# Performance work log

Measured on AMD Instinct MI355X. Metric: run time of the kernel, lower is better.

The kernel has to match this reference:

```python
import jax, jax.numpy as jnp
import numpy as np

C = 256; HEADS = 16; BS = 8; HS = 3; PS = BS + 2 * HS; G = 32; EPS = 1e-5


def gnorm(x, w, b):
    # GroupNorm(32, C) over any (B, C, *) tensor
    B, Ch = x.shape[0], x.shape[1]
    xs = x.reshape(B, G, -1)
    m = xs.mean(-1, keepdims=True)
    v = xs.var(-1, keepdims=True)
    xs = (xs - m) * jax.lax.rsqrt(v + EPS)
    sh = (1, Ch) + (1,) * (x.ndim - 2)
    return xs.reshape(x.shape) * w.reshape(sh) + b.reshape(sh)


def mha(q, k, v, scale):
    attn = jax.nn.softmax(jnp.einsum('bhid,bhjd->bhij', q, k) * scale, axis=-1)
    return jnp.einsum('bhij,bhjd->bhid', attn, v)


def conv1x1(x, w, b=None):
    y = jnp.einsum('bchw,cd->bdhw', x, w)
    return y if b is None else y + b[None, :, None, None]


def spatial_attn(x, w1, b1, w2, b2, gw, gb):
    wgt = jax.nn.relu(conv1x1(x, w1, b1))
    wgt = jax.nn.sigmoid(conv1x1(wgt, w2, b2))
    return gnorm(x * wgt + x, gw, gb)


def halo_attn(x, qkv_w, proj_w, proj_b):
    B, Ch, H, W = x.shape
    pad_h = (-H) % BS; pad_w = (-W) % BS
    xp = jnp.pad(x, ((0, 0), (0, 0), (HS, pad_h + HS), (HS, pad_w + HS)))
    Hb = (H + pad_h) // BS; Wb = (W + pad_w) // BS
    rows = (np.arange(Hb) * BS)[:, None] + np.arange(PS)  # (Hb, PS)
    cols = (np.arange(Wb) * BS)[:, None] + np.arange(PS)  # (Wb, PS)
    # (B, C, Hb, Wb, PS, PS) halo windows, row-major like F.unfold
    p = xp[:, :, rows[:, None, :, None], cols[None, :, None, :]]
    p = p.transpose(0, 2, 3, 4, 5, 1).reshape(B * Hb * Wb, PS * PS, Ch)
    qkv = p @ qkv_w  # (N, P, 3C)
    d = Ch // HEADS
    qkv = qkv.reshape(-1, PS * PS, 3, HEADS, d).transpose(2, 0, 3, 1, 4)
    q, k, v = qkv[0], qkv[1], qkv[2]  # (N, heads, P, d)
    center = np.array([r * PS + c for r in range(HS, HS + BS) for c in range(HS, HS + BS)])
    q = q[:, :, center, :]  # only center block queries
    o = mha(q, k, v, d ** -0.5)  # (N, heads, BS*BS, d)
    o = o.transpose(0, 2, 1, 3).reshape(-1, BS * BS, Ch) @ proj_w + proj_b
    o = o.reshape(B, Hb, Wb, BS, BS, Ch).transpose(0, 5, 1, 3, 2, 4)
    o = o.reshape(B, Ch, H + pad_h, W + pad_w)
    return o[:, :, :H, :W]


def rot_pass(xn, w):
    B, Ch, H, W = xn.shape
    d = Ch // HEADS
    qkv = conv1x1(xn, w).reshape(B, 3, HEADS, d, H * W)
    q = qkv[:, 0].transpose(0, 1, 3, 2)  # (B, heads, HW, d)
    k = qkv[:, 1].transpose(0, 1, 3, 2)
    v = qkv[:, 2].transpose(0, 1, 3, 2)
    o = mha(q, k, v, d ** -0.5)
    return o.transpose(0, 1, 3, 2).reshape(B, Ch, H, W)


def rotation_attn(x, gw, gb, qkv_w, pw, pb):
    xn = gnorm(x, gw, gb)
    outs = [rot_pass(xn, qkv_w)]
    for k in (1, 2, 3):
        o = rot_pass(jnp.rot90(xn, k, axes=(2, 3)), qkv_w)
        outs.append(jnp.rot90(o, 4 - k, axes=(2, 3)))
    m = jnp.maximum(jnp.maximum(outs[0], outs[1]), jnp.maximum(outs[2], outs[3]))
    return conv1x1(m, pw, pb) + x


def setup_inputs() -> dict:
    key = jax.random.key(0)
    ks = jax.random.split(key, 16)
    B, H, W = 2, 32, 32
    n = lambda k, s: jax.random.normal(k, s, dtype=jnp.float32) * 0.05
    return {
        'x': jax.random.normal(ks[0], (B, C, H, W), dtype=jnp.float32),
        'sa_w1': n(ks[1], (C, C // 8)), 'sa_b1': jnp.zeros((C // 8,), jnp.float32),
        'sa_w2': n(ks[2], (C // 8, C)), 'sa_b2': jnp.zeros((C,), jnp.float32),
        'sa_gn_w': jnp.ones((C,), jnp.float32), 'sa_gn_b': jnp.zeros((C,), jnp.float32),
        'ha_qkv_w': n(ks[3], (C, 3 * C)), 'ha_proj_w': n(ks[4], (C, C)), 'ha_proj_b': jnp.zeros((C,), jnp.float32),
        'ra_gn_w': jnp.ones((C,), jnp.float32), 'ra_gn_b': jnp.zeros((C,), jnp.float32),
        'ra_qkv_w': n(ks[5], (C, 3 * C)), 'ra_proj_w': n(ks[6], (C, C)), 'ra_proj_b': jnp.zeros((C,), jnp.float32),
        'gn_w': jnp.ones((C,), jnp.float32), 'gn_b': jnp.zeros((C,), jnp.float32),
        'toqkv_w': n(ks[7], (C, 3 * C)), 'toqkv_b': jnp.zeros((3 * C,), jnp.float32),
        'attn_weight': jnp.ones((4,), jnp.float32),
        'proj_w': n(ks[8], (C, C)), 'proj_b': jnp.zeros((C,), jnp.float32),
    }


def reference(x, sa_w1, sa_b1, sa_w2, sa_b2, sa_gn_w, sa_gn_b,
              ha_qkv_w, ha_proj_w, ha_proj_b,
              ra_gn_w, ra_gn_b, ra_qkv_w, ra_proj_w, ra_proj_b,
              gn_w, gn_b, toqkv_w, toqkv_b, attn_weight, proj_w, proj_b):
    B, Ch, H, W = x.shape
    d = Ch // HEADS
    sp = spatial_attn(x, sa_w1, sa_b1, sa_w2, sa_b2, sa_gn_w, sa_gn_b)
    ha = halo_attn(x, ha_qkv_w, ha_proj_w, ha_proj_b)
    ro = rotation_attn(x, ra_gn_w, ra_gn_b, ra_qkv_w, ra_proj_w, ra_proj_b)
    # global QKV attention over flattened tokens
    nf = gnorm(x.reshape(B, Ch, H * W), gn_w, gn_b).transpose(0, 2, 1)  # (B, HW, C)
    qkv = nf @ toqkv_w + toqkv_b
    q, k, v = jnp.split(qkv, 3, axis=-1)
    q = q.reshape(B, -1, HEADS, d).transpose(0, 2, 1, 3)
    k = k.reshape(B, -1, HEADS, d).transpose(0, 2, 1, 3)
    v = v.reshape(B, -1, HEADS, d).transpose(0, 2, 1, 3)
    o = mha(q, k, v, d ** -0.5).transpose(0, 2, 1, 3).reshape(B, -1, Ch)
    qo = o.transpose(0, 2, 1).reshape(B, Ch, H, W)
    w4 = jax.nn.softmax(attn_weight)
    comb = sp * w4[0] + ha * w4[1] + qo * w4[2] + ro * w4[3]
    return conv1x1(comb, proj_w, proj_b) + x
```

## Files before the change

### kernel.cpp

```cpp
#include <hip/hip_runtime.h>

#define CC 256
#define HWN 1024
#define EPSV 1e-5f

typedef __attribute__((ext_vector_type(8))) short bf16x8;
typedef __attribute__((ext_vector_type(4))) float f32x4;
typedef __attribute__((ext_vector_type(4))) unsigned short u16x4;

__device__ inline ushort f2bf(float f) {
    union { float f; unsigned u; } v; v.f = f;
    unsigned u = v.u;
    u += 0x7fffu + ((u >> 16) & 1u);
    return (ushort)(u >> 16);
}
__device__ inline void store_out(float* p, float v) { *p = v; }
__device__ inline void store_out(ushort* p, float v) { *p = f2bf(v); }

__global__ __launch_bounds__(256) void k_transpose(const float* __restrict__ in,
                                                   float* __restrict__ out, int R, int Cd) {
    __shared__ float tile[32][33];
    int b = blockIdx.z;
    int r0 = blockIdx.y * 32, c0 = blockIdx.x * 32;
    int tx = threadIdx.x, ty = threadIdx.y;
    const float* inb = in + (size_t)b * R * Cd;
    float* outb = out + (size_t)b * R * Cd;
#pragma unroll
    for (int i = 0; i < 32; i += 8)
        tile[ty + i][tx] = inb[(size_t)(r0 + ty + i) * Cd + c0 + tx];
    __syncthreads();
#pragma unroll
    for (int i = 0; i < 32; i += 8)
        outb[(size_t)(c0 + ty + i) * R + r0 + tx] = tile[tx][ty + i];
}

__global__ __launch_bounds__(256) void k_wtc_all(const float* __restrict__ s0, const float* __restrict__ s1,
                                                 const float* __restrict__ s2, const float* __restrict__ s3,
                                                 const float* __restrict__ s4, const float* __restrict__ s5,
                                                 ushort* __restrict__ d0, ushort* __restrict__ d1,
                                                 ushort* __restrict__ d2, ushort* __restrict__ d3,
                                                 ushort* __restrict__ d4, ushort* __restrict__ d5) {
    __shared__ float tile[32][33];
    int z = blockIdx.z;
    const float* in; ushort* out; int N;
    switch (z) {
        case 0: in = s0; out = d0; N = 768; break;
        case 1: in = s1; out = d1; N = 768; break;
        case 2: in = s2; out = d2; N = 768; break;
        case 3: in = s3; out = d3; N = 256; break;
        case 4: in = s4; out = d4; N = 256; break;
        default: in = s5; out = d5; N = 256; break;
    }
    int n0 = blockIdx.x * 32;
    if (n0 >= N) return;
    int k0 = blockIdx.y * 32;
    int tx = threadIdx.x, ty = threadIdx.y;
#pragma unroll
    for (int i = 0; i < 32; i += 8)
        tile[ty + i][tx] = in[(size_t)(k0 + ty + i) * N + n0 + tx];
    __syncthreads();
#pragma unroll
    for (int i = 0; i < 32; i += 8)
        out[(size_t)(n0 + ty + i) * 256 + k0 + tx] = f2bf(tile[tx][ty + i]);
}

template <typename OT>
__global__ __launch_bounds__(256) void k_mm_bf(const float* __restrict__ A,
                                               const ushort* __restrict__ Wt,
                                               const float* __restrict__ bias,
                                               const float* __restrict__ res,
                                               OT* __restrict__ Cp,
                                               int M, int N, int K) {
    __shared__ __align__(16) ushort As[64][40];
    __shared__ __align__(16) ushort Bs[64][40];
    int tid = threadIdx.x;
    int lane = tid & 63, wid = tid >> 6;
    int wr = (wid >> 1) * 32, wc = (wid & 1) * 32;
    int row0 = blockIdx.y * 64, col0 = blockIdx.x * 64;
    int sr = tid >> 2, skq = (tid & 3) * 8;
    int l16 = lane & 15, kg = (lane >> 4) * 8;
    f32x4 acc[2][2] = {};
    for (int k0 = 0; k0 < K; k0 += 32) {
        const float* ap = &A[(size_t)(row0 + sr) * K + k0 + skq];
        float4 a0 = *(const float4*)ap, a1 = *(const float4*)(ap + 4);
        bf16x8 av;
        av[0] = (short)f2bf(a0.x); av[1] = (short)f2bf(a0.y);
        av[2] = (short)f2bf(a0.z); av[3] = (short)f2bf(a0.w);
        av[4] = (short)f2bf(a1.x); av[5] = (short)f2bf(a1.y);
        av[6] = (short)f2bf(a1.z); av[7] = (short)f2bf(a1.w);
        *(bf16x8*)&As[sr][skq] = av;
        *(bf16x8*)&Bs[sr][skq] = *(const bf16x8*)&Wt[(size_t)(col0 + sr) * K + k0 + skq];
        __syncthreads();
        bf16x8 af0 = *(bf16x8*)&As[wr + l16][kg];
        bf16x8 af1 = *(bf16x8*)&As[wr + 16 + l16][kg];
        bf16x8 bf0 = *(bf16x8*)&Bs[wc + l16][kg];
        bf16x8 bf1 = *(bf16x8*)&Bs[wc + 16 + l16][kg];
        acc[0][0] = __builtin_amdgcn_mfma_f32_16x16x32_bf16(af0, bf0, acc[0][0], 0, 0, 0);
        acc[0][1] = __builtin_amdgcn_mfma_f32_16x16x32_bf16(af0, bf1, acc[0][1], 0, 0, 0);
        acc[1][0] = __builtin_amdgcn_mfma_f32_16x16x32_bf16(af1, bf0, acc[1][0], 0, 0, 0);
        acc[1][1] = __builtin_amdgcn_mfma_f32_16x16x32_bf16(af1, bf1, acc[1][1], 0, 0, 0);
        __syncthreads();
    }
#pragma unroll
    for (int fr = 0; fr < 2; fr++)
#pragma unroll
        for (int fc = 0; fc < 2; fc++)
#pragma unroll
            for (int reg = 0; reg < 4; reg++) {
                int r = row0 + wr + fr * 16 + (lane >> 4) * 4 + reg;
                int c = col0 + wc + fc * 16 + l16;
                float v = acc[fr][fc][reg];
                if (bias) v += bias[c];
                if (res) v += res[(size_t)r * N + c];
                store_out(&Cp[(size_t)r * N + c], v);
            }
}

__global__ __launch_bounds__(256) void k_spatial(const float* __restrict__ xT,
                                                 const float* __restrict__ w1,
                                                 const float* __restrict__ b1,
                                                 const float* __restrict__ w2,
                                                 const float* __restrict__ b2,
                                                 float* __restrict__ spre) {
    __shared__ float w1s[8192];
    __shared__ float w2s[8192];
    __shared__ float xs[16][260];
    __shared__ float s1s[16][36];
    int tid = threadIdx.x;
    int tok0 = blockIdx.x * 16;
    {
        const float4* w1v = (const float4*)w1;
        const float4* w2v = (const float4*)w2;
        float4* w1sv = (float4*)w1s;
        float4* w2sv = (float4*)w2s;
        for (int i = tid; i < 2048; i += 256) {
            w1sv[i] = w1v[i];
            w2sv[i] = w2v[i];
        }
        for (int i = tid; i < 1024; i += 256) {
            int tok = i >> 6, part = i & 63;
            *(float4*)&xs[tok][part * 4] =
                *(const float4*)&xT[(size_t)(tok0 + tok) * 256 + part * 4];
        }
    }
    __syncthreads();
    int tok = tid >> 4, col = tid & 15;
    {
        float a0 = b1[col], a1 = b1[col + 16];
        for (int k = 0; k < 256; k++) {
            float xv = xs[tok][k];
            a0 = fmaf(xv, w1s[k * 32 + col], a0);
            a1 = fmaf(xv, w1s[k * 32 + col + 16], a1);
        }
        s1s[tok][col] = fmaxf(a0, 0.f);
        s1s[tok][col + 16] = fmaxf(a1, 0.f);
    }
    __syncthreads();
#pragma unroll 4
    for (int j = 0; j < 16; j++) {
        int c = col + j * 16;
        float a = b2[c];
#pragma unroll
        for (int k = 0; k < 32; k++)
            a = fmaf(s1s[tok][k], w2s[k * 256 + c], a);
        float sg = 1.f / (1.f + __expf(-a));
        spre[(size_t)(tok0 + tok) * 256 + c] = xs[tok][c] * (1.f + sg);
    }
}

__global__ __launch_bounds__(256) void k_gstats(const float* __restrict__ in, float* __restrict__ stats) {
    int bg = blockIdx.x;
    int b = bg >> 5, g = bg & 31;
    int tid = threadIdx.x;
    float s = 0.f, s2 = 0.f;
    for (int idx = tid; idx < HWN * 8; idx += 256) {
        int t = idx >> 3, cc = idx & 7;
        float v = in[(size_t)(b * HWN + t) * CC + g * 8 + cc];
        s += v;
        s2 += v * v;
    }
    __shared__ float sh[2][256];
    sh[0][tid] = s; sh[1][tid] = s2;
    __syncthreads();
    for (int off = 128; off > 0; off >>= 1) {
        if (tid < off) { sh[0][tid] += sh[0][tid + off]; sh[1][tid] += sh[1][tid + off]; }
        __syncthreads();
    }
    if (tid == 0) {
        float mean = sh[0][0] * (1.f / (HWN * 8));
        float var = sh[1][0] * (1.f / (HWN * 8)) - mean * mean;
        stats[bg * 2] = mean;
        stats[bg * 2 + 1] = rsqrtf(var + EPSV);
    }
}

__global__ __launch_bounds__(256) void k_gnorm_apply(const float* __restrict__ in,
                                                     const float* __restrict__ stats,
                                                     const float* __restrict__ w,
                                                     const float* __restrict__ bb,
                                                     float* __restrict__ out) {
    int idx = blockIdx.x * 256 + threadIdx.x;
    int c = idx & 255;
    int t = idx >> 8;
    int b = t >> 10;
    int g = c >> 3;
    float mean = stats[(b * 32 + g) * 2], rstd = stats[(b * 32 + g) * 2 + 1];
    out[idx] = (in[idx] - mean) * rstd * w[c] + bb[c];
}

__global__ __launch_bounds__(256) void k_patch(const float* __restrict__ xT, float* __restrict__ p) {
    int rowid = blockIdx.x;
    int blk = rowid / 196, pos = rowid % 196;
    int b = blk >> 4, hb = (blk >> 2) & 3, wb = blk & 3;
    int i = pos / 14, j = pos % 14;
    int y = hb * 8 + i - 3, xx = wb * 8 + j - 3;
    int c = threadIdx.x;
    float v = 0.f;
    if (y >= 0 && y < 32 && xx >= 0 && xx < 32)
        v = xT[(size_t)(b * HWN + y * 32 + xx) * CC + c];
    p[(size_t)rowid * CC + c] = v;
}

__global__ __launch_bounds__(256, 4) void k_attn_mfma(const ushort* __restrict__ qkv0,
                                                      const ushort* __restrict__ qkv1,
                                                      float* __restrict__ out0,
                                                      float* __restrict__ out1) {
    __shared__ __align__(16) ushort K_lds[32][24];
    __shared__ __align__(16) ushort V_lds[16][40];
    __shared__ __align__(16) ushort P_lds[4][16][40];
    __shared__ float l_sh[4][16];
    int gx = blockIdx.x;
    int src = gx >> 5, bh = gx & 31;
    int b = bh >> 4, h = bh & 15;
    const ushort* qkv = src ? qkv1 : qkv0;
    float* out = src ? out1 : out0;
    int tid = threadIdx.x;
    int lane = tid & 63, wid = tid >> 6;
    int l16 = lane & 15, g = lane >> 4;
    const ushort* base = qkv + (size_t)b * HWN * 768 + h * 16;
    int q0 = blockIdx.y * 64 + wid * 16;
    bf16x8 qf = {};
    if (g < 2)
        qf = *(const bf16x8*)(base + (size_t)(q0 + l16) * 768 + g * 8);
    f32x4 acc = {};
    float lsum = 0.f;
    int skey = tid >> 3, spiece = tid & 7;
    for (int kb = 0; kb < 32; kb++) {
        __syncthreads();
        {
            const ushort* rp = base + (size_t)(kb * 32 + skey) * 768;
            if (spiece < 4) {
                *(u16x4*)&K_lds[skey][spiece * 4] = *(const u16x4*)(rp + 256 + spiece * 4);
            } else {
                int dd = (spiece - 4) * 4;
                u16x4 vv = *(const u16x4*)(rp + 512 + dd);
                V_lds[dd][skey]     = vv[0];
                V_lds[dd + 1][skey] = vv[1];
                V_lds[dd + 2][skey] = vv[2];
                V_lds[dd + 3][skey] = vv[3];
            }
        }
        __syncthreads();
#pragma unroll
        for (int sb = 0; sb < 2; sb++) {
            bf16x8 kf = {};
            if (g < 2)
                kf = *(const bf16x8*)&K_lds[sb * 16 + l16][g * 8];
            f32x4 st = {};
            st = __builtin_amdgcn_mfma_f32_16x16x32_bf16(kf, qf, st, 0, 0, 0);
            float e0 = __expf(st[0] * 0.25f);
            float e1 = __expf(st[1] * 0.25f);
            float e2 = __expf(st[2] * 0.25f);
            float e3 = __expf(st[3] * 0.25f);
            lsum += (e0 + e1) + (e2 + e3);
            u16x4 pp;
            pp[0] = f2bf(e0); pp[1] = f2bf(e1); pp[2] = f2bf(e2); pp[3] = f2bf(e3);
            *(u16x4*)&P_lds[wid][l16][sb * 16 + g * 4] = pp;
        }
        bf16x8 pf = *(const bf16x8*)&P_lds[wid][l16][g * 8];
        bf16x8 vf = *(const bf16x8*)&V_lds[l16][g * 8];
        acc = __builtin_amdgcn_mfma_f32_16x16x32_bf16(pf, vf, acc, 0, 0, 0);
    }
    lsum += __shfl_xor(lsum, 16);
    lsum += __shfl_xor(lsum, 32);
    if (g == 0) l_sh[wid][l16] = lsum;
#pragma unroll
    for (int r = 0; r < 4; r++) {
        float inv = 1.f / l_sh[wid][g * 4 + r];
        out[(size_t)(b * HWN + q0 + g * 4 + r) * CC + h * 16 + l16] = acc[r] * inv;
    }
}

__global__ __launch_bounds__(64) void k_attn_halo(const float* __restrict__ qkv, float* __restrict__ out) {
    int blk = blockIdx.x;
    int h = blockIdx.y;
    int tid = threadIdx.x;
    __shared__ float Ks[196][16];
    __shared__ float Vs[196][16];
    const float* base = qkv + (size_t)blk * 196 * 768 + h * 16;
    for (int idx = tid; idx < 196 * 4; idx += 64) {
        int kk = idx >> 2, part = idx & 3;
        const float* rowp = base + (size_t)kk * 768 + part * 4;
        *(float4*)&Ks[kk][part * 4] = *(const float4*)(rowp + 256);
        *(float4*)&Vs[kk][part * 4] = *(const float4*)(rowp + 512);
    }
    __syncthreads();
    int ci = tid >> 3, cj = tid & 7;
    int cpos = (3 + ci) * 14 + (3 + cj);
    float q[16];
    {
        const float4* qp = (const float4*)(base + (size_t)cpos * 768);
#pragma unroll
        for (int i = 0; i < 4; i++) {
            float4 v = qp[i];
            q[i * 4] = v.x; q[i * 4 + 1] = v.y; q[i * 4 + 2] = v.z; q[i * 4 + 3] = v.w;
        }
    }
    float l = 0.f, acc[16] = {};
    for (int k4 = 0; k4 < 196; k4 += 4) {
        float s[4] = {};
#pragma unroll
        for (int j = 0; j < 4; j++) {
            const float4* kp = (const float4*)&Ks[k4 + j][0];
#pragma unroll
            for (int i = 0; i < 4; i++) {
                float4 kv = kp[i];
                s[j] = fmaf(q[i * 4], kv.x, s[j]);
                s[j] = fmaf(q[i * 4 + 1], kv.y, s[j]);
                s[j] = fmaf(q[i * 4 + 2], kv.z, s[j]);
                s[j] = fmaf(q[i * 4 + 3], kv.w, s[j]);
            }
        }
        float e[4];
#pragma unroll
        for (int j = 0; j < 4; j++) e[j] = __expf(s[j] * 0.25f);
        l += (e[0] + e[1]) + (e[2] + e[3]);
#pragma unroll
        for (int j = 0; j < 4; j++) {
            const float4* vp = (const float4*)&Vs[k4 + j][0];
#pragma unroll
            for (int i = 0; i < 4; i++) {
                float4 vv = vp[i];
                acc[i * 4]     = fmaf(e[j], vv.x, acc[i * 4]);
                acc[i * 4 + 1] = fmaf(e[j], vv.y, acc[i * 4 + 1]);
                acc[i * 4 + 2] = fmaf(e[j], vv.z, acc[i * 4 + 2]);
                acc[i * 4 + 3] = fmaf(e[j], vv.w, acc[i * 4 + 3]);
            }
        }
    }
    float inv = 1.f / l;
    int b = blk >> 4, hb = (blk >> 2) & 3, wb = blk & 3;
    int t = (hb * 8 + ci) * 32 + wb * 8 + cj;
    float4* op = (float4*)(out + (size_t)(b * HWN + t) * CC + h * 16);
#pragma unroll
    for (int i = 0; i < 4; i++)
        op[i] = make_float4(acc[i * 4] * inv, acc[i * 4 + 1] * inv, acc[i * 4 + 2] * inv, acc[i * 4 + 3] * inv);
}

__global__ __launch_bounds__(256) void k_combine(const float* __restrict__ sp, const float* __restrict__ ha,
                                                 const float* __restrict__ qo, const float* __restrict__ ro,
                                                 const float* __restrict__ aw, float* __restrict__ comb) {
    int idx = blockIdx.x * 256 + threadIdx.x;
    float a0 = aw[0], a1 = aw[1], a2 = aw[2], a3 = aw[3];
    float mx = fmaxf(fmaxf(a0, a1), fmaxf(a2, a3));
    float e0 = __expf(a0 - mx), e1 = __expf(a1 - mx), e2 = __expf(a2 - mx), e3 = __expf(a3 - mx);
    float inv = 1.f / (e0 + e1 + e2 + e3);
    comb[idx] = (sp[idx] * e0 + ha[idx] * e1 + qo[idx] * e2 + ro[idx] * e3) * inv;
}

extern "C" void kernel_launch(void* const* d_in, const int* in_sizes, int n_in,
                              void* d_out, int out_size, void* d_ws, size_t ws_size,
                              hipStream_t stream) {
    const float* x        = (const float*)d_in[0];
    const float* sa_w1    = (const float*)d_in[1];
    const float* sa_b1    = (const float*)d_in[2];
    const float* sa_w2    = (const float*)d_in[3];
    const float* sa_b2    = (const float*)d_in[4];
    const float* sa_gn_w  = (const float*)d_in[5];
    const float* sa_gn_b  = (const float*)d_in[6];
    const float* ha_qkv_w = (const float*)d_in[7];
    const float* ha_proj_w= (const float*)d_in[8];
    const float* ha_proj_b= (const float*)d_in[9];
    const float* ra_gn_w  = (const float*)d_in[10];
    const float* ra_gn_b  = (const float*)d_in[11];
    const float* ra_qkv_w = (const float*)d_in[12];
    const float* ra_proj_w= (const float*)d_in[13];
    const float* ra_proj_b= (const float*)d_in[14];
    const float* gn_w     = (const float*)d_in[15];
    const float* gn_b     = (const float*)d_in[16];
    const float* toqkv_w  = (const float*)d_in[17];
    const float* toqkv_b  = (const float*)d_in[18];
    const float* attn_w   = (const float*)d_in[19];
    const float* proj_w   = (const float*)d_in[20];
    const float* proj_b   = (const float*)d_in[21];
    float* out = (float*)d_out;

    float* ws = (float*)d_ws;
    size_t off = 0;
    float* xT   = ws + off; off += 524288;
    float* sp   = ws + off; off += 524288;
    float* xn   = ws + off; off += 524288;
    float* nf   = ws + off; off += 524288;
    float* ha   = ws + off; off += 524288;
    float* ro   = ws + off; off += 524288;
    float* qo   = ws + off; off += 524288;
    float* abuf = ws + off; off += 524288;
    float* stats= ws + off; off += 256;
    float* big0 = ws + off; off += 4816896;
    float* big1 = ws + off; off += 1605632;
    ushort* wt_ha_qkv = (ushort*)(ws + off); off += 98304;
    ushort* wt_ra_qkv = (ushort*)(ws + off); off += 98304;
    ushort* wt_toqkv  = (ushort*)(ws + off); off += 98304;
    ushort* wt_ha_pj  = (ushort*)(ws + off); off += 32768;
    ushort* wt_ra_pj  = (ushort*)(ws + off); off += 32768;
    ushort* wt_pj     = (ushort*)(ws + off); off += 32768;
    float* comb = xn;
    float* otok = nf;
    float* qkv_ha = big0;
    ushort* qkv_ra_bf = (ushort*)big0;
    ushort* qkv_g_bf  = (ushort*)(big0 + 786432);
    float* pbuf = big1;
    float* spre = big1 + 65536;

    dim3 blk256(256), blkT(32, 8);

    k_wtc_all<<<dim3(24, 8, 6), blkT, 0, stream>>>(
        ha_qkv_w, ra_qkv_w, toqkv_w, ha_proj_w, ra_proj_w, proj_w,
        wt_ha_qkv, wt_ra_qkv, wt_toqkv, wt_ha_pj, wt_ra_pj, wt_pj);

    k_transpose<<<dim3(32, 8, 2), blkT, 0, stream>>>(x, xT, 256, 1024);

    k_patch<<<dim3(6272), blk256, 0, stream>>>(xT, pbuf);
    k_mm_bf<float><<<dim3(12, 98), blk256, 0, stream>>>(pbuf, wt_ha_qkv, nullptr, nullptr, qkv_ha, 6272, 768, 256);
    k_attn_halo<<<dim3(32, 16), dim3(64), 0, stream>>>(qkv_ha, abuf);
    k_mm_bf<float><<<dim3(4, 32), blk256, 0, stream>>>(abuf, wt_ha_pj, ha_proj_b, nullptr, ha, 2048, 256, 256);

    k_spatial<<<dim3(128), blk256, 0, stream>>>(xT, sa_w1, sa_b1, sa_w2, sa_b2, spre);
    k_gstats<<<dim3(64), blk256, 0, stream>>>(spre, stats);
    k_gnorm_apply<<<dim3(2048), blk256, 0, stream>>>(spre, stats, sa_gn_w, sa_gn_b, sp);

    k_gstats<<<dim3(64), blk256, 0, stream>>>(xT, stats + 128);
    k_gnorm_apply<<<dim3(2048), blk256, 0, stream>>>(xT, stats + 128, ra_gn_w, ra_gn_b, xn);
    k_gnorm_apply<<<dim3(2048), blk256, 0, stream>>>(xT, stats + 128, gn_w, gn_b, nf);

    k_mm_bf<ushort><<<dim3(12, 32), blk256, 0, stream>>>(xn, wt_ra_qkv, nullptr, nullptr, qkv_ra_bf, 2048, 768, 256);
    k_mm_bf<ushort><<<dim3(12, 32), blk256, 0, stream>>>(nf, wt_toqkv, toqkv_b, nullptr, qkv_g_bf, 2048, 768, 256);
    k_attn_mfma<<<dim3(64, 16), blk256, 0, stream>>>(qkv_ra_bf, qkv_g_bf, abuf, qo);

    k_mm_bf<float><<<dim3(4, 32), blk256, 0, stream>>>(abuf, wt_ra_pj, ra_proj_b, xT, ro, 2048, 256, 256);

    k_combine<<<dim3(2048), blk256, 0, stream>>>(sp, ha, qo, ro, attn_w, comb);
    k_mm_bf<float><<<dim3(4, 32), blk256, 0, stream>>>(comb, wt_pj, proj_b, xT, otok, 2048, 256, 256);
    k_transpose<<<dim3(8, 32, 2), blkT, 0, stream>>>(otok, out, 1024, 256);
}
```

Before: 271.6 us.

## Project halo QKV per token, gather windows in attention, fuse combine and GroupNorm apply

The halo QKV projection now runs once per token (2048 rows) instead of once per padded window position (6272 rows). The attention kernel gathers K/V for each window from that per-token result and writes zeros for positions that fall in the padding, which is valid because the projection has no bias. The softmax-weighted combine of the four branches moves into the A-tile load of the final projection GEMM, and the two GroupNorm applies that share statistics become one kernel. Together these remove the patch kernel, about two thirds of the halo GEMM work, and several full-tensor round trips through memory.

```diff
diff --git a/kernel.cpp b/kernel.cpp
--- a/kernel.cpp
+++ b/kernel.cpp
@@ -116,6 +116,71 @@
             }
 }
 
+__global__ __launch_bounds__(256) void k_mm_comb(const float* __restrict__ sp,
+                                                 const float* __restrict__ hab,
+                                                 const float* __restrict__ qo,
+                                                 const float* __restrict__ ro,
+                                                 const float* __restrict__ aw,
+                                                 const ushort* __restrict__ Wt,
+                                                 const float* __restrict__ bias,
+                                                 const float* __restrict__ res,
+                                                 float* __restrict__ Cp) {
+    __shared__ __align__(16) ushort As[64][40];
+    __shared__ __align__(16) ushort Bs[64][40];
+    const int N = 256, K = 256;
+    int tid = threadIdx.x;
+    int lane = tid & 63, wid = tid >> 6;
+    int wr = (wid >> 1) * 32, wc = (wid & 1) * 32;
+    int row0 = blockIdx.y * 64, col0 = blockIdx.x * 64;
+    int sr = tid >> 2, skq = (tid & 3) * 8;
+    int l16 = lane & 15, kg = (lane >> 4) * 8;
+    float a0 = aw[0], a1 = aw[1], a2 = aw[2], a3 = aw[3];
+    float mx = fmaxf(fmaxf(a0, a1), fmaxf(a2, a3));
+    float e0 = __expf(a0 - mx), e1 = __expf(a1 - mx), e2 = __expf(a2 - mx), e3 = __expf(a3 - mx);
+    float inv = 1.f / (e0 + e1 + e2 + e3);
+    float w0 = e0 * inv, w1 = e1 * inv, w2 = e2 * inv, w3 = e3 * inv;
+    f32x4 acc[2][2] = {};
+    for (int k0 = 0; k0 < K; k0 += 32) {
+        size_t aoff = (size_t)(row0 + sr) * K + k0 + skq;
+        float4 s0 = *(const float4*)&sp[aoff],  s1 = *(const float4*)&sp[aoff + 4];
+        float4 h0 = *(const float4*)&hab[aoff], h1 = *(const float4*)&hab[aoff + 4];
+        float4 q0 = *(const float4*)&qo[aoff],  q1 = *(const float4*)&qo[aoff + 4];
+        float4 r0 = *(const float4*)&ro[aoff],  r1 = *(const float4*)&ro[aoff + 4];
+        bf16x8 av;
+        av[0] = (short)f2bf(w0 * s0.x + w1 * h0.x + w2 * q0.x + w3 * r0.x);
+        av[1] = (short)f2bf(w0 * s0.y + w1 * h0.y + w2 * q0.y + w3 * r0.y);
+        av[2] = (short)f2bf(w0 * s0.z + w1 * h0.z + w2 * q0.z + w3 * r0.z);
+        av[3] = (short)f2bf(w0 * s0.w + w1 * h0.w + w2 * q0.w + w3 * r0.w);
+        av[4] = (short)f2bf(w0 * s1.x + w1 * h1.x + w2 * q1.x + w3 * r1.x);
+        av[5] = (short)f2bf(w0 * s1.y + w1 * h1.y + w2 * q1.y + w3 * r1.y);
+        av[6] = (short)f2bf(w0 * s1.z + w1 * h1.z + w2 * q1.z + w3 * r1.z);
+        av[7] = (short)f2bf(w0 * s1.w + w1 * h1.w + w2 * q1.w + w3 * r1.w);
+        *(bf16x8*)&As[sr][skq] = av;
+        *(bf16x8*)&Bs[sr][skq] = *(const bf16x8*)&Wt[(size_t)(col0 + sr) * K + k0 + skq];
+        __syncthreads();
+        bf16x8 af0 = *(bf16x8*)&As[wr + l16][kg];
+        bf16x8 af1 = *(bf16x8*)&As[wr + 16 + l16][kg];
+        bf16x8 bf0 = *(bf16x8*)&Bs[wc + l16][kg];
+        bf16x8 bf1 = *(bf16x8*)&Bs[wc + 16 + l16][kg];
+        acc[0][0] = __builtin_amdgcn_mfma_f32_16x16x32_bf16(af0, bf0, acc[0][0], 0, 0, 0);
+        acc[0][1] = __builtin_amdgcn_mfma_f32_16x16x32_bf16(af0, bf1, acc[0][1], 0, 0, 0);
+        acc[1][0] = __builtin_amdgcn_mfma_f32_16x16x32_bf16(af1, bf0, acc[1][0], 0, 0, 0);
+        acc[1][1] = __builtin_amdgcn_mfma_f32_16x16x32_bf16(af1, bf1, acc[1][1], 0, 0, 0);
+        __syncthreads();
+    }
+#pragma unroll
+    for (int fr = 0; fr < 2; fr++)
+#pragma unroll
+        for (int fc = 0; fc < 2; fc++)
+#pragma unroll
+            for (int reg = 0; reg < 4; reg++) {
+                int r = row0 + wr + fr * 16 + (lane >> 4) * 4 + reg;
+                int c = col0 + wc + fc * 16 + l16;
+                float v = acc[fr][fc][reg] + bias[c] + res[(size_t)r * N + c];
+                Cp[(size_t)r * N + c] = v;
+            }
+}
+
 __global__ __launch_bounds__(256) void k_spatial(const float* __restrict__ xT,
                                                  const float* __restrict__ w1,
                                                  const float* __restrict__ b1,
@@ -208,17 +273,23 @@
     out[idx] = (in[idx] - mean) * rstd * w[c] + bb[c];
 }
 
-__global__ __launch_bounds__(256) void k_patch(const float* __restrict__ xT, float* __restrict__ p) {
-    int rowid = blockIdx.x;
-    int blk = rowid / 196, pos = rowid % 196;
-    int b = blk >> 4, hb = (blk >> 2) & 3, wb = blk & 3;
-    int i = pos / 14, j = pos % 14;
-    int y = hb * 8 + i - 3, xx = wb * 8 + j - 3;
-    int c = threadIdx.x;
-    float v = 0.f;
-    if (y >= 0 && y < 32 && xx >= 0 && xx < 32)
-        v = xT[(size_t)(b * HWN + y * 32 + xx) * CC + c];
-    p[(size_t)rowid * CC + c] = v;
+__global__ __launch_bounds__(256) void k_gnorm_apply2(const float* __restrict__ in,
+                                                      const float* __restrict__ stats,
+                                                      const float* __restrict__ w1,
+                                                      const float* __restrict__ b1,
+                                                      const float* __restrict__ w2,
+                                                      const float* __restrict__ b2,
+                                                      float* __restrict__ o1,
+                                                      float* __restrict__ o2) {
+    int idx = blockIdx.x * 256 + threadIdx.x;
+    int c = idx & 255;
+    int t = idx >> 8;
+    int b = t >> 10;
+    int g = c >> 3;
+    float mean = stats[(b * 32 + g) * 2], rstd = stats[(b * 32 + g) * 2 + 1];
+    float nrm = (in[idx] - mean) * rstd;
+    o1[idx] = nrm * w1[c] + b1[c];
+    o2[idx] = nrm * w2[c] + b2[c];
 }
 
 __global__ __launch_bounds__(256, 4) void k_attn_mfma(const ushort* __restrict__ qkv0,
@@ -291,25 +362,35 @@
     }
 }
 
-__global__ __launch_bounds__(64) void k_attn_halo(const float* __restrict__ qkv, float* __restrict__ out) {
+__global__ __launch_bounds__(64) void k_attn_halo(const float* __restrict__ qkv_tok,
+                                                  float* __restrict__ out) {
     int blk = blockIdx.x;
     int h = blockIdx.y;
     int tid = threadIdx.x;
     __shared__ float Ks[196][16];
     __shared__ float Vs[196][16];
-    const float* base = qkv + (size_t)blk * 196 * 768 + h * 16;
+    int b = blk >> 4, hb = (blk >> 2) & 3, wb = blk & 3;
+    const float* base = qkv_tok + (size_t)b * HWN * 768;
     for (int idx = tid; idx < 196 * 4; idx += 64) {
         int kk = idx >> 2, part = idx & 3;
-        const float* rowp = base + (size_t)kk * 768 + part * 4;
-        *(float4*)&Ks[kk][part * 4] = *(const float4*)(rowp + 256);
-        *(float4*)&Vs[kk][part * 4] = *(const float4*)(rowp + 512);
+        int i = kk / 14, j = kk % 14;
+        int y = hb * 8 + i - 3, xx = wb * 8 + j - 3;
+        float4 kv = make_float4(0.f, 0.f, 0.f, 0.f);
+        float4 vv = make_float4(0.f, 0.f, 0.f, 0.f);
+        if (y >= 0 && y < 32 && xx >= 0 && xx < 32) {
+            const float* rowp = base + (size_t)(y * 32 + xx) * 768 + h * 16 + part * 4;
+            kv = *(const float4*)(rowp + 256);
+            vv = *(const float4*)(rowp + 512);
+        }
+        *(float4*)&Ks[kk][part * 4] = kv;
+        *(float4*)&Vs[kk][part * 4] = vv;
     }
     __syncthreads();
     int ci = tid >> 3, cj = tid & 7;
-    int cpos = (3 + ci) * 14 + (3 + cj);
+    int tq = (hb * 8 + ci) * 32 + wb * 8 + cj;
     float q[16];
     {
-        const float4* qp = (const float4*)(base + (size_t)cpos * 768);
+        const float4* qp = (const float4*)(base + (size_t)tq * 768 + h * 16);
 #pragma unroll
         for (int i = 0; i < 4; i++) {
             float4 v = qp[i];
@@ -349,23 +430,10 @@
         }
     }
     float inv = 1.f / l;
-    int b = blk >> 4, hb = (blk >> 2) & 3, wb = blk & 3;
-    int t = (hb * 8 + ci) * 32 + wb * 8 + cj;
-    float4* op = (float4*)(out + (size_t)(b * HWN + t) * CC + h * 16);
+    float4* op = (float4*)(out + (size_t)(b * HWN + tq) * CC + h * 16);
 #pragma unroll
     for (int i = 0; i < 4; i++)
         op[i] = make_float4(acc[i * 4] * inv, acc[i * 4 + 1] * inv, acc[i * 4 + 2] * inv, acc[i * 4 + 3] * inv);
-}
-
-__global__ __launch_bounds__(256) void k_combine(const float* __restrict__ sp, const float* __restrict__ ha,
-                                                 const float* __restrict__ qo, const float* __restrict__ ro,
-                                                 const float* __restrict__ aw, float* __restrict__ comb) {
-    int idx = blockIdx.x * 256 + threadIdx.x;
-    float a0 = aw[0], a1 = aw[1], a2 = aw[2], a3 = aw[3];
-    float mx = fmaxf(fmaxf(a0, a1), fmaxf(a2, a3));
-    float e0 = __expf(a0 - mx), e1 = __expf(a1 - mx), e2 = __expf(a2 - mx), e3 = __expf(a3 - mx);
-    float inv = 1.f / (e0 + e1 + e2 + e3);
-    comb[idx] = (sp[idx] * e0 + ha[idx] * e1 + qo[idx] * e2 + ro[idx] * e3) * inv;
 }
 
 extern "C" void kernel_launch(void* const* d_in, const int* in_sizes, int n_in,
@@ -414,13 +482,11 @@
     ushort* wt_ha_pj  = (ushort*)(ws + off); off += 32768;
     ushort* wt_ra_pj  = (ushort*)(ws + off); off += 32768;
     ushort* wt_pj     = (ushort*)(ws + off); off += 32768;
-    float* comb = xn;
     float* otok = nf;
-    float* qkv_ha = big0;
-    ushort* qkv_ra_bf = (ushort*)big0;
-    ushort* qkv_g_bf  = (ushort*)(big0 + 786432);
-    float* pbuf = big1;
-    float* spre = big1 + 65536;
+    float* qkv_tok_ha = big0;
+    ushort* qkv_ra_bf = (ushort*)(big0 + 1572864);
+    ushort* qkv_g_bf  = (ushort*)(big0 + 1572864 + 786432);
+    float* spre = big1;
 
     dim3 blk256(256), blkT(32, 8);
 
@@ -430,9 +496,8 @@
 
     k_transpose<<<dim3(32, 8, 2), blkT, 0, stream>>>(x, xT, 256, 1024);
 
-    k_patch<<<dim3(6272), blk256, 0, stream>>>(xT, pbuf);
-    k_mm_bf<float><<<dim3(12, 98), blk256, 0, stream>>>(pbuf, wt_ha_qkv, nullptr, nullptr, qkv_ha, 6272, 768, 256);
-    k_attn_halo<<<dim3(32, 16), dim3(64), 0, stream>>>(qkv_ha, abuf);
+    k_mm_bf<float><<<dim3(12, 32), blk256, 0, stream>>>(xT, wt_ha_qkv, nullptr, nullptr, qkv_tok_ha, 2048, 768, 256);
+    k_attn_halo<<<dim3(32, 16), dim3(64), 0, stream>>>(qkv_tok_ha, abuf);
     k_mm_bf<float><<<dim3(4, 32), blk256, 0, stream>>>(abuf, wt_ha_pj, ha_proj_b, nullptr, ha, 2048, 256, 256);
 
     k_spatial<<<dim3(128), blk256, 0, stream>>>(xT, sa_w1, sa_b1, sa_w2, sa_b2, spre);
@@ -440,8 +505,7 @@
     k_gnorm_apply<<<dim3(2048), blk256, 0, stream>>>(spre, stats, sa_gn_w, sa_gn_b, sp);
 
     k_gstats<<<dim3(64), blk256, 0, stream>>>(xT, stats + 128);
-    k_gnorm_apply<<<dim3(2048), blk256, 0, stream>>>(xT, stats + 128, ra_gn_w, ra_gn_b, xn);
-    k_gnorm_apply<<<dim3(2048), blk256, 0, stream>>>(xT, stats + 128, gn_w, gn_b, nf);
+    k_gnorm_apply2<<<dim3(2048), blk256, 0, stream>>>(xT, stats + 128, ra_gn_w, ra_gn_b, gn_w, gn_b, xn, nf);
 
     k_mm_bf<ushort><<<dim3(12, 32), blk256, 0, stream>>>(xn, wt_ra_qkv, nullptr, nullptr, qkv_ra_bf, 2048, 768, 256);
     k_mm_bf<ushort><<<dim3(12, 32), blk256, 0, stream>>>(nf, wt_toqkv, toqkv_b, nullptr, qkv_g_bf, 2048, 768, 256);
@@ -449,7 +513,6 @@
 
     k_mm_bf<float><<<dim3(4, 32), blk256, 0, stream>>>(abuf, wt_ra_pj, ra_proj_b, xT, ro, 2048, 256, 256);
 
-    k_combine<<<dim3(2048), blk256, 0, stream>>>(sp, ha, qo, ro, attn_w, comb);
-    k_mm_bf<float><<<dim3(4, 32), blk256, 0, stream>>>(comb, wt_pj, proj_b, xT, otok, 2048, 256, 256);
+    k_mm_comb<<<dim3(4, 32), blk256, 0, stream>>>(sp, ha, qo, ro, attn_w, wt_pj, proj_b, xT, otok);
     k_transpose<<<dim3(8, 32, 2), blkT, 0, stream>>>(otok, out, 1024, 256);
 }
```

Result: faster. 261.7 us (-3.6%).
